# Kernel tuning notes

Measured on AMD Instinct MI355X. Metric: run time of the kernel, lower is better.

Reference implementation:

```python
import jax, jax.numpy as jnp
import numpy as np

B, S, D = 1, 4096, 896
NH, NKV, HD = 14, 2, 64
ROPE_BASE = 1000000.0

def rotate_half(x):
    x1, x2 = x[..., :x.shape[-1] // 2], x[..., x.shape[-1] // 2:]
    return jnp.concatenate((-x2, x1), axis=-1)

def rope_tables(seq_len, head_dim, base):
    inv_freq = 1.0 / (base ** (jnp.arange(0, head_dim, 2, dtype=jnp.float32) / head_dim))
    t = jnp.arange(seq_len, dtype=jnp.float32)
    freqs = jnp.einsum('i,j->ij', t, inv_freq)
    emb = jnp.concatenate((freqs, freqs), axis=-1)  # [S, HD]
    return jnp.cos(emb), jnp.sin(emb)

def setup_inputs() -> dict:
    key = jax.random.key(0)
    ks = jax.random.split(key, 6)
    hidden_states = jax.random.normal(ks[0], (B, S, D), dtype=jnp.float32)
    # additive causal mask [1,1,S,S]
    neg = jnp.finfo(jnp.float32).min
    causal = jnp.where(jnp.tril(jnp.ones((S, S), dtype=bool)), 0.0, neg)
    attention_mask = causal[None, None, :, :].astype(jnp.float32)
    sc = 0.02
    Wq = jax.random.normal(ks[1], (D, NH * HD), dtype=jnp.float32) * sc
    Wk = jax.random.normal(ks[2], (D, NKV * HD), dtype=jnp.float32) * sc
    Wv = jax.random.normal(ks[3], (D, NKV * HD), dtype=jnp.float32) * sc
    Wo = jax.random.normal(ks[4], (D, D), dtype=jnp.float32) * sc
    bq = jnp.zeros((NH * HD,), jnp.float32)
    bk = jnp.zeros((NKV * HD,), jnp.float32)
    bv = jnp.zeros((NKV * HD,), jnp.float32)
    return {"hidden_states": hidden_states, "attention_mask": attention_mask,
            "Wq": Wq, "bq": bq, "Wk": Wk, "bk": bk, "Wv": Wv, "bv": bv, "Wo": Wo}

def reference(hidden_states, attention_mask, Wq, bq, Wk, bk, Wv, bv, Wo):
    b, s, _ = hidden_states.shape
    groups = NH // NKV
    q = (hidden_states @ Wq + bq).reshape(b, s, NH, HD)
    k = (hidden_states @ Wk + bk).reshape(b, s, NKV, HD)
    v = (hidden_states @ Wv + bv).reshape(b, s, NKV, HD)
    cos, sin = rope_tables(s, HD, ROPE_BASE)
    cos = cos[None, :, None, :]
    sin = sin[None, :, None, :]
    q = q * cos + rotate_half(q) * sin
    k = k * cos + rotate_half(k) * sin
    # GQA: repeat KV heads
    k = jnp.repeat(k, groups, axis=2)
    v = jnp.repeat(v, groups, axis=2)
    # [b, h, s, d]
    q = jnp.transpose(q, (0, 2, 1, 3))
    k = jnp.transpose(k, (0, 2, 1, 3))
    v = jnp.transpose(v, (0, 2, 1, 3))
    attn = jnp.einsum('bhqd,bhkd->bhqk', q, k) / jnp.sqrt(jnp.float32(HD))
    attn = attn + attention_mask
    attn = jax.nn.softmax(attn, axis=-1)
    out = jnp.einsum('bhqk,bhkd->bhqd', attn, v)
    out = jnp.transpose(out, (0, 2, 1, 3)).reshape(b, s, NH * HD)
    return out @ Wo
```

## Files before the change

### kernel.cpp

```cpp
#include <hip/hip_runtime.h>
#include <math.h>

constexpr int S_    = 4096;
constexpr int Dm    = 896;
constexpr int NHd   = 14;
constexpr int NKVh  = 2;
constexpr int HDim  = 64;
constexpr int NQ    = NHd * HDim;
constexpr int NK    = NKVh * HDim;
constexpr int NQK   = NQ + NK;
constexpr int GROUPS = NHd / NKVh;
constexpr float L2B   = 19.9315685693241740873f;
constexpr float LOG2E = 1.44269504088896340736f;

typedef __attribute__((ext_vector_type(8))) short bf16x8;
typedef __attribute__((ext_vector_type(4))) short bf16x4;
typedef __attribute__((ext_vector_type(4))) float f32x4;
typedef __attribute__((ext_vector_type(2))) int   i32x2;

__device__ __forceinline__ short f2bf(float f) {
  unsigned u = __builtin_bit_cast(unsigned, f);
  unsigned r = (u + 0x7FFFu + ((u >> 16) & 1u)) >> 16;
  return (short)r;
}
__device__ __forceinline__ float bf2f(short s) {
  return __builtin_bit_cast(float, ((unsigned)(unsigned short)s) << 16);
}

__device__ __forceinline__ int cvtpk(float lo, float hi) {
  int r;
  asm("v_cvt_pk_bf16_f32 %0, %1, %2" : "=v"(r) : "v"(lo), "v"(hi));
  return r;
}

__device__ __forceinline__ void gload16(const void* g, void* l) {
  __builtin_amdgcn_global_load_lds(
      (const __attribute__((address_space(1))) unsigned int*)g,
      (__attribute__((address_space(3))) unsigned int*)l, 16, 0, 0);
}

__global__ __launch_bounds__(256) void prep_small(
    const float* __restrict__ hs, short* __restrict__ hsb,
    float* __restrict__ cost, float* __restrict__ sint)
{
  int bid = blockIdx.x;
  if (bid < 1792) {
    int idx = bid * 256 + threadIdx.x;
    float4 a = ((const float4*)hs)[idx * 2];
    float4 b = ((const float4*)hs)[idx * 2 + 1];
    bf16x8 o;
    o[0] = f2bf(a.x); o[1] = f2bf(a.y); o[2] = f2bf(a.z); o[3] = f2bf(a.w);
    o[4] = f2bf(b.x); o[5] = f2bf(b.y); o[6] = f2bf(b.z); o[7] = f2bf(b.w);
    ((bf16x8*)hsb)[idx] = o;
  } else {
    int idx = (bid - 1792) * 256 + threadIdx.x;
    int m = idx >> 5, j = idx & 31;
    float invf = exp2f(-(float)j * (L2B / 32.0f));
    float th = (float)m * invf;
    float s, c;
    sincosf(th, &s, &c);
    cost[idx] = c;
    sint[idx] = s;
  }
}

__global__ __launch_bounds__(256) void transpose_all(
    const float* __restrict__ Wq, const float* __restrict__ Wk,
    const float* __restrict__ Wv, const float* __restrict__ Wo,
    short* __restrict__ wtq, short* __restrict__ wto)
{
  __shared__ float t[64 * 68];
  const int kt = blockIdx.x;
  const int by = blockIdx.y;
  const int tid = threadIdx.x;

  const float* src; int srcN, nt; short* dst; int rowOff;
  if (by < 14)      { src = Wq; srcN = NQ; nt = by;      dst = wtq; rowOff = 0; }
  else if (by < 16) { src = Wk; srcN = NK; nt = by - 14; dst = wtq; rowOff = 896; }
  else if (by < 18) { src = Wv; srcN = NK; nt = by - 16; dst = wtq; rowOff = 1024; }
  else              { src = Wo; srcN = NQ; nt = by - 18; dst = wto; rowOff = 0; }

  #pragma unroll
  for (int i = 0; i < 4; i++) {
    int idx = tid + i * 256;
    int r = idx >> 4, c4 = (idx & 15) * 4;
    *(float4*)&t[r * 68 + c4] =
        *(const float4*)&src[(size_t)(kt * 64 + r) * srcN + nt * 64 + c4];
  }
  __syncthreads();
  const int nl = tid >> 2;
  const int kc = (tid & 3) * 16;
  bf16x8 o0, o1;
  #pragma unroll
  for (int i = 0; i < 8; i++) o0[i] = f2bf(t[(kc + i) * 68 + nl]);
  #pragma unroll
  for (int i = 0; i < 8; i++) o1[i] = f2bf(t[(kc + 8 + i) * 68 + nl]);
  short* dp = dst + (size_t)(rowOff + nt * 64 + nl) * 896 + kt * 64 + kc;
  *(bf16x8*)dp = o0;
  *(bf16x8*)(dp + 8) = o1;
}

template<int EPI>
__global__ __launch_bounds__(256) void gemm128(
    const short* __restrict__ A, const short* __restrict__ Bt,
    const float* __restrict__ biasq, const float* __restrict__ biask,
    const float* __restrict__ biasv,
    const float* __restrict__ cost, const float* __restrict__ sint,
    short* __restrict__ qkb, short* __restrict__ vtb,
    float* __restrict__ outp)
{
  __shared__ short Als[128 * 64];
  __shared__ short Bls[128 * 64];
  const int tid = threadIdx.x;
  const int lane = tid & 63;
  const int w = tid >> 6;
  const int wm = w >> 1, wn = w & 1;
  const int r16 = lane & 15, rg = lane >> 4;
  const int bm = blockIdx.x, bn = blockIdx.y;

  const f32x4 zero4 = {0.f, 0.f, 0.f, 0.f};
  f32x4 acc[4][4];
  #pragma unroll
  for (int mt = 0; mt < 4; mt++)
    #pragma unroll
    for (int nt = 0; nt < 4; nt++) acc[mt][nt] = zero4;

  const int srow = (lane >> 3);
  const int scol = (lane & 7) * 8;

  for (int kt = 0; kt < 14; ++kt) {
    __syncthreads();
    #pragma unroll
    for (int i = 0; i < 4; i++) {
      int c = i * 4 + w;
      int row = c * 8 + srow;
      gload16(A  + (size_t)(bm * 128 + row) * 896 + kt * 64 + scol, &Als[c * 512]);
      gload16(Bt + (size_t)(bn * 128 + row) * 896 + kt * 64 + scol, &Bls[c * 512]);
    }
    __syncthreads();

    bf16x8 af[4][2], bfr[4][2];
    #pragma unroll
    for (int mt = 0; mt < 4; mt++)
      #pragma unroll
      for (int ks = 0; ks < 2; ks++)
        af[mt][ks] = *(const bf16x8*)&Als[(wm * 64 + mt * 16 + r16) * 64 + ks * 32 + rg * 8];
    #pragma unroll
    for (int nt = 0; nt < 4; nt++)
      #pragma unroll
      for (int ks = 0; ks < 2; ks++)
        bfr[nt][ks] = *(const bf16x8*)&Bls[(wn * 64 + nt * 16 + r16) * 64 + ks * 32 + rg * 8];
    #pragma unroll
    for (int mt = 0; mt < 4; mt++)
      #pragma unroll
      for (int nt = 0; nt < 4; nt++)
        #pragma unroll
        for (int ks = 0; ks < 2; ks++)
          acc[mt][nt] = __builtin_amdgcn_mfma_f32_16x16x32_bf16(
              af[mt][ks], bfr[nt][ks], acc[mt][nt], 0, 0, 0);
  }

  if (EPI == 0) {
    const int nbase = bn * 128 + wn * 64;
    if (bn < 8) {
      const float scl = (bn < 7) ? (0.125f * LOG2E) : 1.0f;
      const float* bias = (bn < 7) ? biasq : (biask - 896);
      #pragma unroll
      for (int mt = 0; mt < 4; mt++) {
        const int m0 = bm * 128 + wm * 64 + mt * 16 + rg * 4;
        #pragma unroll
        for (int nt = 0; nt < 4; nt++) {
          int n = nbase + nt * 16 + r16;
          int j = n & 31;
          float sgn = (n & 32) ? 1.f : -1.f;
          float b0 = bias[n], b1 = bias[n ^ 32];
          #pragma unroll
          for (int r = 0; r < 4; r++) {
            int m = m0 + r;
            float c_ = cost[m * 32 + j], s_ = sint[m * 32 + j];
            float val = ((acc[mt][nt][r] + b0) * c_ +
                         sgn * (acc[mt][nt ^ 2][r] + b1) * s_) * scl;
            qkb[(size_t)m * NQK + n] = f2bf(val);
          }
        }
      }
    } else {
      #pragma unroll
      for (int mt = 0; mt < 4; mt++) {
        const int m0 = bm * 128 + wm * 64 + mt * 16 + rg * 4;
        #pragma unroll
        for (int nt = 0; nt < 4; nt++) {
          int vc = wn * 64 + nt * 16 + r16;
          float b0 = biasv[vc];
          bf16x4 pk;
          #pragma unroll
          for (int r = 0; r < 4; r++) pk[r] = f2bf(acc[mt][nt][r] + b0);
          *(bf16x4*)&vtb[(size_t)vc * S_ + m0] = pk;
        }
      }
    }
  } else {
    #pragma unroll
    for (int mt = 0; mt < 4; mt++) {
      const int m0 = bm * 128 + wm * 64 + mt * 16 + rg * 4;
      #pragma unroll
      for (int nt = 0; nt < 4; nt++) {
        int n = bn * 128 + wn * 64 + nt * 16 + r16;
        #pragma unroll
        for (int r = 0; r < 4; r++)
          outp[(size_t)(m0 + r) * NQ + n] = acc[mt][nt][r];
      }
    }
  }
}

__global__ __launch_bounds__(256, 4) void flash_mfma(
    const short* __restrict__ qkb, const short* __restrict__ vtb,
    short* __restrict__ attnb, short* __restrict__ orec,
    float* __restrict__ mlrec)
{
  __shared__ __align__(16) char lds[51200];

  const int tid  = threadIdx.x;
  const int lane = tid & 63;
  const int w    = tid >> 6;
  const int r16  = lane & 15;
  const int rg   = lane >> 4;
  const int bid  = blockIdx.x;
  const int h    = bid % 14;
  const int e    = bid / 14;

  int qt, kt_lo, kt_hi, recid;
  if (e < 32) {
    qt = 31 - (e >> 1);
    int s = e & 1;
    kt_lo = s * (qt + 1);
    kt_hi = kt_lo + (qt + 1);
    recid = (h * 16 + (qt - 16)) * 2 + s;
  } else {
    qt = 47 - e;
    kt_lo = 0;
    kt_hi = 2 * qt + 2;
    recid = -1;
  }
  const int kv = h / GROUPS;
  const int q0 = qt * 128;
  char* Pw = lds + 32768 + w * 4608;
  const int kbase2 = (NQ + kv * HDim) * 2;

  const char* qkbB = (const char*)qkb;
  const char* vtbB = (const char*)vtb;
  const int c8   = tid & 7;
  const int key0 = tid >> 3;
  const int key1 = key0 + 32;
  const char* ksrc0 = qkbB + (size_t)(kt_lo * 64 + key0) * 2048 + kbase2 + ((c8 ^ (key0 & 7)) << 4);
  const char* ksrc1 = qkbB + (size_t)(kt_lo * 64 + key1) * 2048 + kbase2 + ((c8 ^ (key1 & 7)) << 4);
  const char* vsrc0 = vtbB + (size_t)(kv * 64 + key0) * 8192 + (size_t)kt_lo * 128 + ((c8 ^ (key0 & 7)) << 4);
  const char* vsrc1 = vtbB + (size_t)(kv * 64 + key1) * 8192 + (size_t)kt_lo * 128 + ((c8 ^ (key1 & 7)) << 4);

  bf16x8 aq[2][2];
  #pragma unroll
  for (int mt = 0; mt < 2; ++mt) {
    const short* qp = qkb + (size_t)(q0 + w * 32 + mt * 16 + r16) * NQK + h * HDim + rg * 8;
    aq[mt][0] = *(const bf16x8*)qp;
    aq[mt][1] = *(const bf16x8*)(qp + 32);
  }

  const f32x4 zero4 = {0.f, 0.f, 0.f, 0.f};
  f32x4 acc_o[2][4];
  f32x4 acc_l[2];
  float mrow[2] = {0.f, 0.f};
  #pragma unroll
  for (int mt = 0; mt < 2; mt++) {
    acc_l[mt] = zero4;
    #pragma unroll
    for (int nt = 0; nt < 4; nt++) acc_o[mt][nt] = zero4;
  }

  bf16x8 ones;
  #pragma unroll
  for (int j = 0; j < 8; j++) ones[j] = (short)0x3F80;

  {
    char* Kb = lds;
    char* Vb = lds + 8192;
    gload16(ksrc0, Kb + w * 1024);
    gload16(ksrc1, Kb + 4096 + w * 1024);
    gload16(vsrc0, Vb + w * 1024);
    gload16(vsrc1, Vb + 4096 + w * 1024);
    ksrc0 += 131072; ksrc1 += 131072;
    vsrc0 += 128;    vsrc1 += 128;
  }

  for (int kt = kt_lo; kt < kt_hi; ++kt) {
    const int cur = (kt - kt_lo) & 1;
    asm volatile("s_waitcnt vmcnt(0)" ::: "memory");
    __builtin_amdgcn_s_barrier();
    if (kt + 1 < kt_hi) {
      char* Kb = lds + ((cur ^ 1) << 14);
      char* Vb = Kb + 8192;
      gload16(ksrc0, Kb + w * 1024);
      gload16(ksrc1, Kb + 4096 + w * 1024);
      gload16(vsrc0, Vb + w * 1024);
      gload16(vsrc1, Vb + 4096 + w * 1024);
      ksrc0 += 131072; ksrc1 += 131072;
      vsrc0 += 128;    vsrc1 += 128;
    }
    __builtin_amdgcn_sched_barrier(0);
    const char* KsB = lds + (cur << 14);
    const char* VtB = KsB + 8192;

    f32x4 sc[2][4];
    #pragma unroll
    for (int mt = 0; mt < 2; mt++)
      #pragma unroll
      for (int nt = 0; nt < 4; nt++) sc[mt][nt] = zero4;
    #pragma unroll
    for (int nt = 0; nt < 4; ++nt) {
      int key = nt * 16 + r16;
      #pragma unroll
      for (int ks = 0; ks < 2; ++ks) {
        bf16x8 bk = *(const bf16x8*)(KsB + key * 128 + (((ks * 4 + rg) ^ (key & 7)) << 4));
        sc[0][nt] = __builtin_amdgcn_mfma_f32_16x16x32_bf16(bk, aq[0][ks], sc[0][nt], 0, 0, 0);
        sc[1][nt] = __builtin_amdgcn_mfma_f32_16x16x32_bf16(bk, aq[1][ks], sc[1][nt], 0, 0, 0);
      }
    }

    #pragma unroll
    for (int mt = 0; mt < 2; ++mt) {
      const int rowmin = q0 + w * 32 + mt * 16;
      if (kt * 64 + 63 > rowmin) {
        const int qg = rowmin + r16;
        #pragma unroll
        for (int nt = 0; nt < 4; nt++) {
          int kg = kt * 64 + nt * 16 + rg * 4;
          #pragma unroll
          for (int r = 0; r < 4; r++)
            sc[mt][nt][r] = (kg + r > qg) ? -1e30f : sc[mt][nt][r];
        }
      }
      float pm = -3e38f;
      #pragma unroll
      for (int nt = 0; nt < 4; nt++)
        #pragma unroll
        for (int r = 0; r < 4; r++) pm = fmaxf(pm, sc[mt][nt][r]);
      pm = fmaxf(pm, __shfl_xor(pm, 16, 64));
      pm = fmaxf(pm, __shfl_xor(pm, 32, 64));

      if (!__all(pm <= mrow[mt] + 8.0f)) {
        float newm = fmaxf(mrow[mt], pm);
        float scl = exp2f(mrow[mt] - newm);
        mrow[mt] = newm;
        acc_l[mt][0] *= scl;
        #pragma unroll
        for (int nt = 0; nt < 4; nt++) {
          acc_o[mt][nt][0] *= scl; acc_o[mt][nt][1] *= scl;
          acc_o[mt][nt][2] *= scl; acc_o[mt][nt][3] *= scl;
        }
      }
      #pragma unroll
      for (int nt = 0; nt < 4; nt++) {
        float p0 = exp2f(sc[mt][nt][0] - mrow[mt]);
        float p1 = exp2f(sc[mt][nt][1] - mrow[mt]);
        float p2 = exp2f(sc[mt][nt][2] - mrow[mt]);
        float p3 = exp2f(sc[mt][nt][3] - mrow[mt]);
        i32x2 pk2 = { cvtpk(p0, p1), cvtpk(p2, p3) };
        *(i32x2*)(Pw + mt * 2304 + r16 * 144 + nt * 32 + rg * 8) = pk2;
      }
    }

    #pragma unroll
    for (int ks = 0; ks < 2; ++ks) {
      bf16x8 pb0 = *(const bf16x8*)(Pw +        r16 * 144 + ks * 64 + rg * 16);
      bf16x8 pb1 = *(const bf16x8*)(Pw + 2304 + r16 * 144 + ks * 64 + rg * 16);
      acc_l[0] = __builtin_amdgcn_mfma_f32_16x16x32_bf16(ones, pb0, acc_l[0], 0, 0, 0);
      acc_l[1] = __builtin_amdgcn_mfma_f32_16x16x32_bf16(ones, pb1, acc_l[1], 0, 0, 0);
      #pragma unroll
      for (int nt = 0; nt < 4; ++nt) {
        int d = nt * 16 + r16;
        bf16x8 av = *(const bf16x8*)(VtB + d * 128 + (((ks * 4 + rg) ^ (d & 7)) << 4));
        acc_o[0][nt] = __builtin_amdgcn_mfma_f32_16x16x32_bf16(av, pb0, acc_o[0][nt], 0, 0, 0);
        acc_o[1][nt] = __builtin_amdgcn_mfma_f32_16x16x32_bf16(av, pb1, acc_o[1][nt], 0, 0, 0);
      }
    }
  }

  if (recid < 0) {
    #pragma unroll
    for (int mt = 0; mt < 2; mt++) {
      float inv = 1.0f / acc_l[mt][0];
      int qg = q0 + w * 32 + mt * 16 + r16;
      short* op = attnb + (size_t)qg * NQ + h * HDim + rg * 4;
      #pragma unroll
      for (int nt = 0; nt < 4; nt++) {
        bf16x4 pk;
        pk[0] = f2bf(acc_o[mt][nt][0] * inv);
        pk[1] = f2bf(acc_o[mt][nt][1] * inv);
        pk[2] = f2bf(acc_o[mt][nt][2] * inv);
        pk[3] = f2bf(acc_o[mt][nt][3] * inv);
        *(bf16x4*)(op + nt * 16) = pk;
      }
    }
  } else {
    short* orp = orec + (size_t)recid * 8192;
    #pragma unroll
    for (int mt = 0; mt < 2; mt++) {
      int qloc = w * 32 + mt * 16 + r16;
      #pragma unroll
      for (int nt = 0; nt < 4; nt++) {
        bf16x4 pk;
        pk[0] = f2bf(acc_o[mt][nt][0]);
        pk[1] = f2bf(acc_o[mt][nt][1]);
        pk[2] = f2bf(acc_o[mt][nt][2]);
        pk[3] = f2bf(acc_o[mt][nt][3]);
        *(bf16x4*)(orp + qloc * 64 + nt * 16 + rg * 4) = pk;
      }
      if (rg == 0) {
        float2 ml = {mrow[mt], acc_l[mt][0]};
        *(float2*)(mlrec + ((size_t)recid * 128 + qloc) * 2) = ml;
      }
    }
  }
}

__global__ __launch_bounds__(256) void merge_halves(
    const short* __restrict__ orec, const float* __restrict__ mlrec,
    short* __restrict__ attnb)
{
  const int u = blockIdx.x;
  const int h = u >> 4;
  const int qt = 16 + (u & 15);
  const int tid = threadIdx.x;
  const int qloc = tid >> 1;
  const int d0 = (tid & 1) * 32;

  float2 ml1 = *(const float2*)(mlrec + ((size_t)(u * 2 + 0) * 128 + qloc) * 2);
  float2 ml2 = *(const float2*)(mlrec + ((size_t)(u * 2 + 1) * 128 + qloc) * 2);
  float M  = fmaxf(ml1.x, ml2.x);
  float a1 = exp2f(ml1.x - M), a2 = exp2f(ml2.x - M);
  float inv = 1.0f / (a1 * ml1.y + a2 * ml2.y);
  float s1 = a1 * inv, s2 = a2 * inv;

  const short* O1 = orec + (size_t)(u * 2 + 0) * 8192 + qloc * 64 + d0;
  const short* O2 = orec + (size_t)(u * 2 + 1) * 8192 + qloc * 64 + d0;
  short* op = attnb + (size_t)(qt * 128 + qloc) * NQ + h * HDim + d0;
  #pragma unroll
  for (int i = 0; i < 4; i++) {
    bf16x8 x1 = *(const bf16x8*)(O1 + i * 8);
    bf16x8 x2 = *(const bf16x8*)(O2 + i * 8);
    bf16x8 o;
    #pragma unroll
    for (int j = 0; j < 8; j++)
      o[j] = f2bf(s1 * bf2f(x1[j]) + s2 * bf2f(x2[j]));
    *(bf16x8*)(op + i * 8) = o;
  }
}

extern "C" void kernel_launch(void* const* d_in, const int* in_sizes, int n_in,
                              void* d_out, int out_size, void* d_ws, size_t ws_size,
                              hipStream_t stream)
{
  const float* hs = (const float*)d_in[0];
  const float* Wq = (const float*)d_in[2];
  const float* bq = (const float*)d_in[3];
  const float* Wk = (const float*)d_in[4];
  const float* bk = (const float*)d_in[5];
  const float* Wv = (const float*)d_in[6];
  const float* bv = (const float*)d_in[7];
  const float* Wo = (const float*)d_in[8];

  short* hsb  = (short*)d_ws;
  short* wtq  = hsb + (size_t)S_ * Dm;
  short* wto  = wtq + (size_t)1152 * 896;
  float* cost = (float*)(wto + (size_t)896 * 896);
  float* sint = cost + (size_t)S_ * 32;
  short* qkb  = (short*)(sint + (size_t)S_ * 32);
  short* vtb  = qkb + (size_t)S_ * NQK;
  short* attnb= vtb + (size_t)NK * S_;
  float* out  = (float*)d_out;

  short* orec  = hsb;
  float* mlrec = (float*)wtq;

  hipLaunchKernelGGL(prep_small, dim3(2304), dim3(256), 0, stream, hs, hsb, cost, sint);
  hipLaunchKernelGGL(transpose_all, dim3(14, 32), dim3(256), 0, stream,
                     Wq, Wk, Wv, Wo, wtq, wto);
  hipLaunchKernelGGL((gemm128<0>), dim3(32, 9), dim3(256), 0, stream,
                     hsb, wtq, bq, bk, bv, cost, sint, qkb, vtb, (float*)nullptr);
  hipLaunchKernelGGL(flash_mfma, dim3(672), dim3(256), 0, stream,
                     qkb, vtb, attnb, orec, mlrec);
  hipLaunchKernelGGL(merge_halves, dim3(224), dim3(256), 0, stream,
                     orec, mlrec, attnb);
  hipLaunchKernelGGL((gemm128<1>), dim3(32, 7), dim3(256), 0, stream,
                     attnb, wto, bq, bk, bv, cost, sint,
                     (short*)nullptr, (short*)nullptr, out);
}
```

Before: 160.8 us.

## Use 256-row query tiles with persistent atomic work queue in flash attention

Doubles the query tile to 256 rows (64 per wave), so each K/V tile loaded into LDS is reused across twice as many query rows. The fixed grid is replaced by 512 persistent blocks that pull work units from an atomic counter, ordered largest-first, with split-KV halves for the longer query tiles. The first split half now writes directly into the output and the merge runs in place, which removes one scratch record. The cost is higher register pressure, since occupancy is lowered to 2 blocks per CU, plus an extra memset and the atomic scheduling overhead.

```diff
diff --git a/kernel.cpp b/kernel.cpp
--- a/kernel.cpp
+++ b/kernel.cpp
@@ -12,6 +12,8 @@
 constexpr int GROUPS = NHd / NKVh;
 constexpr float L2B   = 19.9315685693241740873f;
 constexpr float LOG2E = 1.44269504088896340736f;
+
+constexpr int NUNITS = 392;
 
 typedef __attribute__((ext_vector_type(8))) short bf16x8;
 typedef __attribute__((ext_vector_type(4))) short bf16x4;
@@ -214,210 +216,223 @@
   }
 }
 
-__global__ __launch_bounds__(256, 4) void flash_mfma(
+__global__ __launch_bounds__(256, 2) void flash_mfma(
     const short* __restrict__ qkb, const short* __restrict__ vtb,
     short* __restrict__ attnb, short* __restrict__ orec,
-    float* __restrict__ mlrec)
+    float* __restrict__ mlrec, unsigned* __restrict__ cnt)
 {
-  __shared__ __align__(16) char lds[51200];
+  __shared__ __align__(16) char lds[65536];
+  __shared__ int s_unit;
 
   const int tid  = threadIdx.x;
   const int lane = tid & 63;
   const int w    = tid >> 6;
   const int r16  = lane & 15;
   const int rg   = lane >> 4;
-  const int bid  = blockIdx.x;
-  const int h    = bid % 14;
-  const int e    = bid / 14;
-
-  int qt, kt_lo, kt_hi, recid;
-  if (e < 32) {
-    qt = 31 - (e >> 1);
-    int s = e & 1;
-    kt_lo = s * (qt + 1);
-    kt_hi = kt_lo + (qt + 1);
-    recid = (h * 16 + (qt - 16)) * 2 + s;
-  } else {
-    qt = 47 - e;
-    kt_lo = 0;
-    kt_hi = 2 * qt + 2;
-    recid = -1;
-  }
-  const int kv = h / GROUPS;
-  const int q0 = qt * 128;
-  char* Pw = lds + 32768 + w * 4608;
-  const int kbase2 = (NQ + kv * HDim) * 2;
-
-  const char* qkbB = (const char*)qkb;
-  const char* vtbB = (const char*)vtb;
+  char* Pw = lds + 32768 + w * 8192;
+
   const int c8   = tid & 7;
   const int key0 = tid >> 3;
   const int key1 = key0 + 32;
-  const char* ksrc0 = qkbB + (size_t)(kt_lo * 64 + key0) * 2048 + kbase2 + ((c8 ^ (key0 & 7)) << 4);
-  const char* ksrc1 = qkbB + (size_t)(kt_lo * 64 + key1) * 2048 + kbase2 + ((c8 ^ (key1 & 7)) << 4);
-  const char* vsrc0 = vtbB + (size_t)(kv * 64 + key0) * 8192 + (size_t)kt_lo * 128 + ((c8 ^ (key0 & 7)) << 4);
-  const char* vsrc1 = vtbB + (size_t)(kv * 64 + key1) * 8192 + (size_t)kt_lo * 128 + ((c8 ^ (key1 & 7)) << 4);
-
-  bf16x8 aq[2][2];
-  #pragma unroll
-  for (int mt = 0; mt < 2; ++mt) {
-    const short* qp = qkb + (size_t)(q0 + w * 32 + mt * 16 + r16) * NQK + h * HDim + rg * 8;
-    aq[mt][0] = *(const bf16x8*)qp;
-    aq[mt][1] = *(const bf16x8*)(qp + 32);
-  }
-
-  const f32x4 zero4 = {0.f, 0.f, 0.f, 0.f};
-  f32x4 acc_o[2][4];
-  f32x4 acc_l[2];
-  float mrow[2] = {0.f, 0.f};
-  #pragma unroll
-  for (int mt = 0; mt < 2; mt++) {
-    acc_l[mt] = zero4;
-    #pragma unroll
-    for (int nt = 0; nt < 4; nt++) acc_o[mt][nt] = zero4;
-  }
+  const int swz0 = (c8 ^ (key0 & 7)) << 4;
+  const int swz1 = (c8 ^ (key1 & 7)) << 4;
 
   bf16x8 ones;
   #pragma unroll
   for (int j = 0; j < 8; j++) ones[j] = (short)0x3F80;
-
-  {
-    char* Kb = lds;
-    char* Vb = lds + 8192;
-    gload16(ksrc0, Kb + w * 1024);
-    gload16(ksrc1, Kb + 4096 + w * 1024);
-    gload16(vsrc0, Vb + w * 1024);
-    gload16(vsrc1, Vb + 4096 + w * 1024);
+  const f32x4 zero4 = {0.f, 0.f, 0.f, 0.f};
+
+  for (;;) {
+    __syncthreads();
+    if (tid == 0) s_unit = (int)atomicAdd(cnt, 1u);
+    __syncthreads();
+    const int u = s_unit;
+    if (u >= NUNITS) break;
+
+    const int e = u / 14;
+    const int h = u - e * 14;
+    int qt, kt_lo, kt_hi, sidx;
+    if (e < 24) {
+      qt = 15 - (e >> 1);
+      sidx = e & 1;
+      const int half = 2 * (qt + 1);
+      kt_lo = sidx * half;
+      kt_hi = kt_lo + half;
+    } else {
+      qt = 27 - e;
+      sidx = -1;
+      kt_lo = 0;
+      kt_hi = 4 * qt + 4;
+    }
+    const int kv = h / GROUPS;
+    const int q0 = qt * 256;
+    const int kbase2 = (NQ + kv * HDim) * 2;
+
+    const char* ksrc0 = (const char*)qkb + (size_t)(kt_lo * 64 + key0) * 2048 + kbase2 + swz0;
+    const char* ksrc1 = (const char*)qkb + (size_t)(kt_lo * 64 + key1) * 2048 + kbase2 + swz1;
+    const char* vsrc0 = (const char*)vtb + (size_t)(kv * 64 + key0) * 8192 + (size_t)kt_lo * 128 + swz0;
+    const char* vsrc1 = (const char*)vtb + (size_t)(kv * 64 + key1) * 8192 + (size_t)kt_lo * 128 + swz1;
+
+    bf16x8 aq[4][2];
+    #pragma unroll
+    for (int mt = 0; mt < 4; ++mt) {
+      const short* qp = qkb + (size_t)(q0 + w * 64 + mt * 16 + r16) * NQK + h * HDim + rg * 8;
+      aq[mt][0] = *(const bf16x8*)qp;
+      aq[mt][1] = *(const bf16x8*)(qp + 32);
+    }
+
+    f32x4 acc_o[4][4];
+    f32x4 acc_l[4];
+    float mrow[4] = {0.f, 0.f, 0.f, 0.f};
+    #pragma unroll
+    for (int mt = 0; mt < 4; mt++) {
+      acc_l[mt] = zero4;
+      #pragma unroll
+      for (int nt = 0; nt < 4; nt++) acc_o[mt][nt] = zero4;
+    }
+
+    gload16(ksrc0, lds + w * 1024);
+    gload16(ksrc1, lds + 4096 + w * 1024);
+    gload16(vsrc0, lds + 8192 + w * 1024);
+    gload16(vsrc1, lds + 12288 + w * 1024);
     ksrc0 += 131072; ksrc1 += 131072;
     vsrc0 += 128;    vsrc1 += 128;
-  }
-
-  for (int kt = kt_lo; kt < kt_hi; ++kt) {
-    const int cur = (kt - kt_lo) & 1;
-    asm volatile("s_waitcnt vmcnt(0)" ::: "memory");
-    __builtin_amdgcn_s_barrier();
-    if (kt + 1 < kt_hi) {
-      char* Kb = lds + ((cur ^ 1) << 14);
-      char* Vb = Kb + 8192;
-      gload16(ksrc0, Kb + w * 1024);
-      gload16(ksrc1, Kb + 4096 + w * 1024);
-      gload16(vsrc0, Vb + w * 1024);
-      gload16(vsrc1, Vb + 4096 + w * 1024);
-      ksrc0 += 131072; ksrc1 += 131072;
-      vsrc0 += 128;    vsrc1 += 128;
-    }
-    __builtin_amdgcn_sched_barrier(0);
-    const char* KsB = lds + (cur << 14);
-    const char* VtB = KsB + 8192;
-
-    f32x4 sc[2][4];
-    #pragma unroll
-    for (int mt = 0; mt < 2; mt++)
-      #pragma unroll
-      for (int nt = 0; nt < 4; nt++) sc[mt][nt] = zero4;
-    #pragma unroll
-    for (int nt = 0; nt < 4; ++nt) {
-      int key = nt * 16 + r16;
+
+    for (int kt = kt_lo; kt < kt_hi; ++kt) {
+      const int cur = (kt - kt_lo) & 1;
+      asm volatile("s_waitcnt vmcnt(0)" ::: "memory");
+      __builtin_amdgcn_s_barrier();
+      if (kt + 1 < kt_hi) {
+        char* Kb = lds + ((cur ^ 1) << 14);
+        gload16(ksrc0, Kb + w * 1024);
+        gload16(ksrc1, Kb + 4096 + w * 1024);
+        gload16(vsrc0, Kb + 8192 + w * 1024);
+        gload16(vsrc1, Kb + 12288 + w * 1024);
+        ksrc0 += 131072; ksrc1 += 131072;
+        vsrc0 += 128;    vsrc1 += 128;
+      }
+      __builtin_amdgcn_sched_barrier(0);
+      const char* KsB = lds + (cur << 14);
+      const char* VtB = KsB + 8192;
+
+      f32x4 sc[4][4];
+      #pragma unroll
+      for (int mt = 0; mt < 4; mt++)
+        #pragma unroll
+        for (int nt = 0; nt < 4; nt++) sc[mt][nt] = zero4;
+      #pragma unroll
+      for (int nt = 0; nt < 4; ++nt) {
+        int key = nt * 16 + r16;
+        #pragma unroll
+        for (int ks = 0; ks < 2; ++ks) {
+          bf16x8 bk = *(const bf16x8*)(KsB + key * 128 + (((ks * 4 + rg) ^ (key & 7)) << 4));
+          #pragma unroll
+          for (int mt = 0; mt < 4; mt++)
+            sc[mt][nt] = __builtin_amdgcn_mfma_f32_16x16x32_bf16(bk, aq[mt][ks], sc[mt][nt], 0, 0, 0);
+        }
+      }
+
+      #pragma unroll
+      for (int mt = 0; mt < 4; ++mt) {
+        const int rowmin = q0 + w * 64 + mt * 16;
+        if (kt * 64 + 63 > rowmin) {
+          const int qg = rowmin + r16;
+          #pragma unroll
+          for (int nt = 0; nt < 4; nt++) {
+            int kg = kt * 64 + nt * 16 + rg * 4;
+            #pragma unroll
+            for (int r = 0; r < 4; r++)
+              sc[mt][nt][r] = (kg + r > qg) ? -1e30f : sc[mt][nt][r];
+          }
+        }
+        float pm = -3e38f;
+        #pragma unroll
+        for (int nt = 0; nt < 4; nt++)
+          #pragma unroll
+          for (int r = 0; r < 4; r++) pm = fmaxf(pm, sc[mt][nt][r]);
+        pm = fmaxf(pm, __shfl_xor(pm, 16, 64));
+        pm = fmaxf(pm, __shfl_xor(pm, 32, 64));
+
+        if (!__all(pm <= mrow[mt] + 8.0f)) {
+          float newm = fmaxf(mrow[mt], pm);
+          float scl = exp2f(mrow[mt] - newm);
+          mrow[mt] = newm;
+          acc_l[mt] *= scl;
+          #pragma unroll
+          for (int nt = 0; nt < 4; nt++) acc_o[mt][nt] *= scl;
+        }
+        #pragma unroll
+        for (int nt = 0; nt < 4; nt++) {
+          float p0 = exp2f(sc[mt][nt][0] - mrow[mt]);
+          float p1 = exp2f(sc[mt][nt][1] - mrow[mt]);
+          float p2 = exp2f(sc[mt][nt][2] - mrow[mt]);
+          float p3 = exp2f(sc[mt][nt][3] - mrow[mt]);
+          i32x2 pk2 = { cvtpk(p0, p1), cvtpk(p2, p3) };
+          *(i32x2*)(Pw + mt * 2048 + r16 * 128 +
+                    ((nt * 32 + rg * 8) ^ ((r16 & 7) << 4))) = pk2;
+        }
+      }
+
       #pragma unroll
       for (int ks = 0; ks < 2; ++ks) {
-        bf16x8 bk = *(const bf16x8*)(KsB + key * 128 + (((ks * 4 + rg) ^ (key & 7)) << 4));
-        sc[0][nt] = __builtin_amdgcn_mfma_f32_16x16x32_bf16(bk, aq[0][ks], sc[0][nt], 0, 0, 0);
-        sc[1][nt] = __builtin_amdgcn_mfma_f32_16x16x32_bf16(bk, aq[1][ks], sc[1][nt], 0, 0, 0);
-      }
-    }
-
-    #pragma unroll
-    for (int mt = 0; mt < 2; ++mt) {
-      const int rowmin = q0 + w * 32 + mt * 16;
-      if (kt * 64 + 63 > rowmin) {
-        const int qg = rowmin + r16;
+        bf16x8 pb[4];
+        #pragma unroll
+        for (int mt = 0; mt < 4; mt++)
+          pb[mt] = *(const bf16x8*)(Pw + mt * 2048 + r16 * 128 +
+                     (((ks * 4 + rg) ^ (r16 & 7)) << 4));
+        #pragma unroll
+        for (int mt = 0; mt < 4; mt++)
+          acc_l[mt] = __builtin_amdgcn_mfma_f32_16x16x32_bf16(ones, pb[mt], acc_l[mt], 0, 0, 0);
+        #pragma unroll
+        for (int nt = 0; nt < 4; ++nt) {
+          int d = nt * 16 + r16;
+          bf16x8 av = *(const bf16x8*)(VtB + d * 128 + (((ks * 4 + rg) ^ (d & 7)) << 4));
+          #pragma unroll
+          for (int mt = 0; mt < 4; mt++)
+            acc_o[mt][nt] = __builtin_amdgcn_mfma_f32_16x16x32_bf16(av, pb[mt], acc_o[mt][nt], 0, 0, 0);
+        }
+      }
+    }
+
+    if (sidx < 0) {
+      #pragma unroll
+      for (int mt = 0; mt < 4; mt++) {
+        float inv = 1.0f / acc_l[mt][0];
+        int qg = q0 + w * 64 + mt * 16 + r16;
+        short* op = attnb + (size_t)qg * NQ + h * HDim + rg * 4;
         #pragma unroll
         for (int nt = 0; nt < 4; nt++) {
-          int kg = kt * 64 + nt * 16 + rg * 4;
-          #pragma unroll
-          for (int r = 0; r < 4; r++)
-            sc[mt][nt][r] = (kg + r > qg) ? -1e30f : sc[mt][nt][r];
-        }
-      }
-      float pm = -3e38f;
-      #pragma unroll
-      for (int nt = 0; nt < 4; nt++)
-        #pragma unroll
-        for (int r = 0; r < 4; r++) pm = fmaxf(pm, sc[mt][nt][r]);
-      pm = fmaxf(pm, __shfl_xor(pm, 16, 64));
-      pm = fmaxf(pm, __shfl_xor(pm, 32, 64));
-
-      if (!__all(pm <= mrow[mt] + 8.0f)) {
-        float newm = fmaxf(mrow[mt], pm);
-        float scl = exp2f(mrow[mt] - newm);
-        mrow[mt] = newm;
-        acc_l[mt][0] *= scl;
+          bf16x4 pk;
+          pk[0] = f2bf(acc_o[mt][nt][0] * inv);
+          pk[1] = f2bf(acc_o[mt][nt][1] * inv);
+          pk[2] = f2bf(acc_o[mt][nt][2] * inv);
+          pk[3] = f2bf(acc_o[mt][nt][3] * inv);
+          *(bf16x4*)(op + nt * 16) = pk;
+        }
+      }
+    } else {
+      const int t = h * 12 + (qt - 4);
+      #pragma unroll
+      for (int mt = 0; mt < 4; mt++) {
+        int qloc = w * 64 + mt * 16 + r16;
+        short* op;
+        if (sidx == 0)
+          op = attnb + (size_t)(q0 + qloc) * NQ + h * HDim + rg * 4;
+        else
+          op = orec + (size_t)t * 16384 + qloc * 64 + rg * 4;
         #pragma unroll
         for (int nt = 0; nt < 4; nt++) {
-          acc_o[mt][nt][0] *= scl; acc_o[mt][nt][1] *= scl;
-          acc_o[mt][nt][2] *= scl; acc_o[mt][nt][3] *= scl;
-        }
-      }
-      #pragma unroll
-      for (int nt = 0; nt < 4; nt++) {
-        float p0 = exp2f(sc[mt][nt][0] - mrow[mt]);
-        float p1 = exp2f(sc[mt][nt][1] - mrow[mt]);
-        float p2 = exp2f(sc[mt][nt][2] - mrow[mt]);
-        float p3 = exp2f(sc[mt][nt][3] - mrow[mt]);
-        i32x2 pk2 = { cvtpk(p0, p1), cvtpk(p2, p3) };
-        *(i32x2*)(Pw + mt * 2304 + r16 * 144 + nt * 32 + rg * 8) = pk2;
-      }
-    }
-
-    #pragma unroll
-    for (int ks = 0; ks < 2; ++ks) {
-      bf16x8 pb0 = *(const bf16x8*)(Pw +        r16 * 144 + ks * 64 + rg * 16);
-      bf16x8 pb1 = *(const bf16x8*)(Pw + 2304 + r16 * 144 + ks * 64 + rg * 16);
-      acc_l[0] = __builtin_amdgcn_mfma_f32_16x16x32_bf16(ones, pb0, acc_l[0], 0, 0, 0);
-      acc_l[1] = __builtin_amdgcn_mfma_f32_16x16x32_bf16(ones, pb1, acc_l[1], 0, 0, 0);
-      #pragma unroll
-      for (int nt = 0; nt < 4; ++nt) {
-        int d = nt * 16 + r16;
-        bf16x8 av = *(const bf16x8*)(VtB + d * 128 + (((ks * 4 + rg) ^ (d & 7)) << 4));
-        acc_o[0][nt] = __builtin_amdgcn_mfma_f32_16x16x32_bf16(av, pb0, acc_o[0][nt], 0, 0, 0);
-        acc_o[1][nt] = __builtin_amdgcn_mfma_f32_16x16x32_bf16(av, pb1, acc_o[1][nt], 0, 0, 0);
-      }
-    }
-  }
-
-  if (recid < 0) {
-    #pragma unroll
-    for (int mt = 0; mt < 2; mt++) {
-      float inv = 1.0f / acc_l[mt][0];
-      int qg = q0 + w * 32 + mt * 16 + r16;
-      short* op = attnb + (size_t)qg * NQ + h * HDim + rg * 4;
-      #pragma unroll
-      for (int nt = 0; nt < 4; nt++) {
-        bf16x4 pk;
-        pk[0] = f2bf(acc_o[mt][nt][0] * inv);
-        pk[1] = f2bf(acc_o[mt][nt][1] * inv);
-        pk[2] = f2bf(acc_o[mt][nt][2] * inv);
-        pk[3] = f2bf(acc_o[mt][nt][3] * inv);
-        *(bf16x4*)(op + nt * 16) = pk;
-      }
-    }
-  } else {
-    short* orp = orec + (size_t)recid * 8192;
-    #pragma unroll
-    for (int mt = 0; mt < 2; mt++) {
-      int qloc = w * 32 + mt * 16 + r16;
-      #pragma unroll
-      for (int nt = 0; nt < 4; nt++) {
-        bf16x4 pk;
-        pk[0] = f2bf(acc_o[mt][nt][0]);
-        pk[1] = f2bf(acc_o[mt][nt][1]);
-        pk[2] = f2bf(acc_o[mt][nt][2]);
-        pk[3] = f2bf(acc_o[mt][nt][3]);
-        *(bf16x4*)(orp + qloc * 64 + nt * 16 + rg * 4) = pk;
-      }
-      if (rg == 0) {
-        float2 ml = {mrow[mt], acc_l[mt][0]};
-        *(float2*)(mlrec + ((size_t)recid * 128 + qloc) * 2) = ml;
+          bf16x4 pk;
+          pk[0] = f2bf(acc_o[mt][nt][0]);
+          pk[1] = f2bf(acc_o[mt][nt][1]);
+          pk[2] = f2bf(acc_o[mt][nt][2]);
+          pk[3] = f2bf(acc_o[mt][nt][3]);
+          *(bf16x4*)(op + nt * 16) = pk;
+        }
+        if (rg == 0) {
+          float2 ml = {mrow[mt], acc_l[mt][0]};
+          *(float2*)(mlrec + ((size_t)(t * 2 + sidx) * 256 + qloc) * 2) = ml;
+        }
       }
     }
   }
@@ -427,32 +442,29 @@
     const short* __restrict__ orec, const float* __restrict__ mlrec,
     short* __restrict__ attnb)
 {
-  const int u = blockIdx.x;
-  const int h = u >> 4;
-  const int qt = 16 + (u & 15);
-  const int tid = threadIdx.x;
-  const int qloc = tid >> 1;
-  const int d0 = (tid & 1) * 32;
-
-  float2 ml1 = *(const float2*)(mlrec + ((size_t)(u * 2 + 0) * 128 + qloc) * 2);
-  float2 ml2 = *(const float2*)(mlrec + ((size_t)(u * 2 + 1) * 128 + qloc) * 2);
+  const int t = blockIdx.x;
+  const int h = t / 12;
+  const int qt = 4 + (t - h * 12);
+  const int qloc = threadIdx.x;
+
+  float2 ml1 = *(const float2*)(mlrec + ((size_t)(t * 2 + 0) * 256 + qloc) * 2);
+  float2 ml2 = *(const float2*)(mlrec + ((size_t)(t * 2 + 1) * 256 + qloc) * 2);
   float M  = fmaxf(ml1.x, ml2.x);
   float a1 = exp2f(ml1.x - M), a2 = exp2f(ml2.x - M);
   float inv = 1.0f / (a1 * ml1.y + a2 * ml2.y);
   float s1 = a1 * inv, s2 = a2 * inv;
 
-  const short* O1 = orec + (size_t)(u * 2 + 0) * 8192 + qloc * 64 + d0;
-  const short* O2 = orec + (size_t)(u * 2 + 1) * 8192 + qloc * 64 + d0;
-  short* op = attnb + (size_t)(qt * 128 + qloc) * NQ + h * HDim + d0;
+  short* O1 = attnb + (size_t)(qt * 256 + qloc) * NQ + h * HDim;
+  const short* O2 = orec + (size_t)t * 16384 + qloc * 64;
   #pragma unroll
-  for (int i = 0; i < 4; i++) {
+  for (int i = 0; i < 8; i++) {
     bf16x8 x1 = *(const bf16x8*)(O1 + i * 8);
     bf16x8 x2 = *(const bf16x8*)(O2 + i * 8);
     bf16x8 o;
     #pragma unroll
     for (int j = 0; j < 8; j++)
       o[j] = f2bf(s1 * bf2f(x1[j]) + s2 * bf2f(x2[j]));
-    *(bf16x8*)(op + i * 8) = o;
+    *(bf16x8*)(O1 + i * 8) = o;
   }
 }
 
@@ -479,17 +491,19 @@
   short* attnb= vtb + (size_t)NK * S_;
   float* out  = (float*)d_out;
 
-  short* orec  = hsb;
-  float* mlrec = (float*)wtq;
+  short*    orec  = hsb;
+  float*    mlrec = cost;
+  unsigned* cnt   = (unsigned*)((char*)attnb + (size_t)S_ * NQ * 2);
 
   hipLaunchKernelGGL(prep_small, dim3(2304), dim3(256), 0, stream, hs, hsb, cost, sint);
   hipLaunchKernelGGL(transpose_all, dim3(14, 32), dim3(256), 0, stream,
                      Wq, Wk, Wv, Wo, wtq, wto);
   hipLaunchKernelGGL((gemm128<0>), dim3(32, 9), dim3(256), 0, stream,
                      hsb, wtq, bq, bk, bv, cost, sint, qkb, vtb, (float*)nullptr);
-  hipLaunchKernelGGL(flash_mfma, dim3(672), dim3(256), 0, stream,
-                     qkb, vtb, attnb, orec, mlrec);
-  hipLaunchKernelGGL(merge_halves, dim3(224), dim3(256), 0, stream,
+  hipMemsetAsync(cnt, 0, 4, stream);
+  hipLaunchKernelGGL(flash_mfma, dim3(512), dim3(256), 0, stream,
+                     qkb, vtb, attnb, orec, mlrec, cnt);
+  hipLaunchKernelGGL(merge_halves, dim3(168), dim3(256), 0, stream,
                      orec, mlrec, attnb);
   hipLaunchKernelGGL((gemm128<1>), dim3(32, 7), dim3(256), 0, stream,
                      attnb, wto, bq, bk, bv, cost, sint,
```

Result: slower. 179.1 us (+11.4%).
